# Kernel tuning notes

Hardware: AMD Instinct MI355X
Metric: run time of the kernel (lower is better)

## Reference

```python
import jax, jax.numpy as jnp
import numpy as np

B, S, DIM = 4, 2048, 1024
H, DH = 16, 64
INNER = H * DH  # 1024
SCALE = DH ** -0.5
NEG = -10000.0


def setup_inputs() -> dict:
    key = jax.random.key(0)
    k1, k2, k3, k4 = jax.random.split(key, 4)
    x = jax.random.normal(k1, (B, S, DIM), dtype=jnp.float32)
    w_qkv = jax.random.normal(k2, (DIM, 3 * INNER), dtype=jnp.float32) * (DIM ** -0.5)
    w_out = jax.random.normal(k3, (INNER, DIM), dtype=jnp.float32) * (INNER ** -0.5)
    b_out = jax.random.normal(k4, (DIM,), dtype=jnp.float32) * 0.01
    return {"x": x, "w_qkv": w_qkv, "w_out": w_out, "b_out": b_out}


def reference(x, w_qkv, w_out, b_out):
    b, s, _ = x.shape
    qkv = x @ w_qkv                                  # [b, s, 3*inner]
    q, k, v = jnp.split(qkv, 3, axis=-1)
    def heads(t):
        return t.reshape(b, s, H, DH).transpose(0, 2, 1, 3)  # [b, h, s, dh]
    q, k, v = heads(q), heads(k), heads(v)
    sim = jnp.einsum('bhid,bhjd->bhij', q, k)        # [b, h, s, s]
    i = jnp.arange(s)
    mask = jnp.where(i[None, :] <= i[:, None], 0.0, NEG).astype(sim.dtype)
    # NOTE: original scales (sim + mask), so mask bias is -10000*scale
    attn = jax.nn.softmax((sim + mask) * SCALE, axis=-1)
    out = jnp.einsum('bhij,bhjd->bhid', attn, v)     # [b, h, s, dh]
    out = out.transpose(0, 2, 1, 3).reshape(b, s, INNER)
    return out @ w_out + b_out
```

## Files before the change

kernel.cpp:

```cpp
#include <hip/hip_runtime.h>
#include <stdint.h>

typedef unsigned short u16;
typedef uint32_t u32;
typedef __attribute__((ext_vector_type(4))) float f32x4;
typedef __attribute__((ext_vector_type(16))) float f32x16;
typedef __attribute__((ext_vector_type(8))) short bf16x8;
typedef __attribute__((ext_vector_type(4))) u32 u32x4;

#define MFMA16(a,b,c) __builtin_amdgcn_mfma_f32_16x16x32_bf16((a),(b),(c),0,0,0)
#define MFMA32(a,b,c) __builtin_amdgcn_mfma_f32_32x32x16_bf16((a),(b),(c),0,0,0)
#define QSCALE 0.18033688011112042f
#define MASKB  -1803.3688011112042f
#define MBASE  -16.0f

__device__ __forceinline__ u16 f2bf(float f){
  union { float f; uint32_t u; } v; v.f = f;
  uint32_t r = v.u + 0x7fffu + ((v.u >> 16) & 1u);
  return (u16)(r >> 16);
}

__device__ __forceinline__ u32 cvtpk(float lo, float hi){
  u32 r;
  asm volatile("v_cvt_pk_bf16_f32 %0, %1, %2" : "=v"(r) : "v"(lo), "v"(hi));
  return r;
}

__device__ __forceinline__ void plswap(u32 &a, u32 &b){
  auto r = __builtin_amdgcn_permlane32_swap(a, b, false, false);
  union { decltype(r) v; u32 w[2]; } u; u.v = r;
  a = u.w[0]; b = u.w[1];
}

union U4 { u32x4 u; bf16x8 b; };
__device__ __forceinline__ bf16x8 mkfrag(u32 a, u32 b, u32 c, u32 d){
  U4 x; x.u = (u32x4){a,b,c,d}; return x.b;
}

__device__ __forceinline__ void gload16(const void* g, void* l){
  __builtin_amdgcn_global_load_lds(
      (const __attribute__((address_space(1))) void*)g,
      (__attribute__((address_space(3))) void*)l, 16, 0, 0);
}

__global__ __launch_bounds__(256) void cvt_bf16_k(const float* __restrict__ in, u16* __restrict__ out){
  int i = blockIdx.x*256 + threadIdx.x;
  float4 v = reinterpret_cast<const float4*>(in)[i];
  ushort4 o;
  o.x = f2bf(v.x); o.y = f2bf(v.y); o.z = f2bf(v.z); o.w = f2bf(v.w);
  reinterpret_cast<ushort4*>(out)[i] = o;
}

__global__ __launch_bounds__(256) void transpose_cvt_k(const float* __restrict__ in, u16* __restrict__ out,
                                                       int R, int C){
  __shared__ float tile[64][65];
  int c0 = blockIdx.x*64, r0 = blockIdx.y*64;
  int t = threadIdx.x; int cc = t & 63, rr = t >> 6;
  #pragma unroll
  for (int i=0;i<16;++i){ int r = rr + i*4; tile[r][cc] = in[(size_t)(r0+r)*C + c0+cc]; }
  __syncthreads();
  #pragma unroll
  for (int i=0;i<16;++i){ int r = rr + i*4; out[(size_t)(c0+r)*R + r0+cc] = f2bf(tile[cc][r]); }
}

__device__ __forceinline__ void gemm_core(const u16* __restrict__ A, const u16* __restrict__ Bt,
                                          int bm, int bn, char* lds, f32x4 (&acc)[4][4]){
  const int K = 1024;
  int tid = threadIdx.x, w = tid >> 6, l = tid & 63;
  int lrow = l & 15, lg = l >> 4;
  int wm = w >> 1, wn = w & 1;
  const u16* aSrc = A + (size_t)(bm*128 + w*32 + (l>>3))*K + (((l&7)^(l>>3))<<3);
  const u16* bSrc = Bt + (size_t)(bn*128 + w*32 + (l>>3))*K + (((l&7)^(l>>3))<<3);
  char* aDst = lds + w*4096;
  char* bDst = lds + 16384 + w*4096;
  for (int kk = 0; kk < 16; ++kk){
    __syncthreads();
    #pragma unroll
    for (int i=0;i<4;++i) gload16(aSrc + (size_t)i*8*K + kk*64, aDst + i*1024);
    #pragma unroll
    for (int i=0;i<4;++i) gload16(bSrc + (size_t)i*8*K + kk*64, bDst + i*1024);
    __syncthreads();
    #pragma unroll
    for (int ks=0; ks<2; ++ks){
      bf16x8 af[4], bfv[4];
      #pragma unroll
      for (int m=0;m<4;++m){
        int row = wm*64 + m*16 + lrow;
        af[m] = *reinterpret_cast<const bf16x8*>(lds + row*128 + (((ks*4+lg)^(row&7))<<4));
      }
      #pragma unroll
      for (int n=0;n<4;++n){
        int row = wn*64 + n*16 + lrow;
        bfv[n] = *reinterpret_cast<const bf16x8*>(lds + 16384 + row*128 + (((ks*4+lg)^(row&7))<<4));
      }
      #pragma unroll
      for (int m=0;m<4;++m){
        #pragma unroll
        for (int n=0;n<4;++n)
          acc[m][n] = MFMA16(af[m], bfv[n], acc[m][n]);
      }
    }
  }
}

__global__ __launch_bounds__(256,4) void gemm_qkv_k(const u16* __restrict__ A, const u16* __restrict__ Bt,
                                                    u16* __restrict__ qw, u16* __restrict__ kw,
                                                    u16* __restrict__ vtw){
  __shared__ __align__(16) char lds[32768];
  f32x4 acc[4][4];
  #pragma unroll
  for (int m=0;m<4;++m){
    #pragma unroll
    for (int n=0;n<4;++n) acc[m][n] = (f32x4){0.f,0.f,0.f,0.f};
  }
  int id = blockIdx.x + 24*blockIdx.y;
  int xcd = id & 7, s = id >> 3;
  int cb = s / 48, r = s % 48;
  int bm = xcd*8 + r/6;
  int bn = cb*6 + r%6;
  gemm_core(A, Bt, bm, bn, lds, acc);
  int tid = threadIdx.x, w = tid >> 6, l = tid & 63;
  int lrow = l & 15, lg = l >> 4;
  int wm = w >> 1, wn = w & 1;
  const int which = bn >> 3;
  if (which < 2){
    #pragma unroll
    for (int n=0;n<4;++n){
      int gcol = bn*128 + wn*64 + n*16 + lrow;
      int inner = gcol & 1023;
      int h = inner >> 6, d = inner & 63;
      #pragma unroll
      for (int m=0;m<4;++m){
        #pragma unroll
        for (int r2=0;r2<4;++r2){
          int grow = bm*128 + wm*64 + m*16 + lg*4 + r2;
          int b = grow >> 11, sq = grow & 2047;
          float v = acc[m][n][r2];
          if (which == 0)
            qw[((size_t)((b*16 + h)*2048 + sq))*64 + d] = f2bf(v * QSCALE);
          else
            kw[((size_t)((b*16 + h)*2048 + sq))*64 + d] = f2bf(v);
        }
      }
    }
  } else {
    __syncthreads();
    #pragma unroll
    for (int n=0;n<4;++n){
      int colL = wn*64 + n*16 + lrow;
      int swz = (colL & 7) << 4;
      #pragma unroll
      for (int m=0;m<4;++m){
        int rowL0 = wm*64 + m*16 + lg*4;
        ushort4 p;
        p.x = f2bf(acc[m][n][0]); p.y = f2bf(acc[m][n][1]);
        p.z = f2bf(acc[m][n][2]); p.w = f2bf(acc[m][n][3]);
        *reinterpret_cast<ushort4*>(lds + colL*256 + ((rowL0*2) ^ swz)) = p;
      }
    }
    __syncthreads();
    const int h0 = bn*2 - 32;
    const int grow0 = bm*128;
    const int b = grow0 >> 11, sq0 = grow0 & 2047;
    const int dp = tid >> 1;
    const int half = (tid & 1) * 128;
    const int h = h0 + (dp >> 6), d = dp & 63;
    const int swz = (dp & 7) << 4;
    u16* dst = vtw + ((size_t)((b*16 + h)*64 + d))*2048 + sq0 + half/2;
    #pragma unroll
    for (int i=0;i<8;++i){
      u32x4 v = *reinterpret_cast<const u32x4*>(lds + dp*256 + ((half + i*16) ^ swz));
      *reinterpret_cast<u32x4*>(dst + i*8) = v;
    }
  }
}

__global__ __launch_bounds__(256) void attn_k(const u16* __restrict__ Qw, const u16* __restrict__ Kw,
                                              const u16* __restrict__ VTw, u16* __restrict__ Ow){
  __shared__ __align__(16) char lds[32768];
  const int bh = blockIdx.x;
  const int y = blockIdx.y, yk = y >> 2, ya = y & 3;
  const int qb = (yk == 0) ? (15 - ya) : (yk == 1) ? (8 + ya) : (yk == 2) ? (4 + ya) : (3 - ya);
  const int tid = threadIdx.x, w = tid >> 6, l = tid & 63;
  const int lo = l & 31, hi = l >> 5;
  const size_t base = (size_t)bh * (2048*64);
  const int qw0 = qb*128 + w*32;
  const int q_l = qw0 + lo;

  bf16x8 qa[4];
  {
    const u16* qsrc = Qw + base + (size_t)q_l*64 + hi*8;
    #pragma unroll
    for (int ks=0; ks<4; ++ks) qa[ks] = *reinterpret_cast<const bf16x8*>(qsrc + ks*16);
  }

  const u32 ONE2 = 0x3F803F80u;
  const bf16x8 onesf = mkfrag(ONE2, ONE2, ONE2, ONE2);

  const int srow = tid >> 3;
  const int scs  = (tid & 7) ^ (srow & 7);
  const u16* kS = Kw  + base + (size_t)srow*64   + scs*8;
  const u16* vS = VTw + base + (size_t)srow*2048 + scs*8;

  f32x16 acc0 = {0,0,0,0,0,0,0,0,0,0,0,0,0,0,0,0};
  f32x16 acc1 = {0,0,0,0,0,0,0,0,0,0,0,0,0,0,0,0};
  f32x16 ls   = {0,0,0,0,0,0,0,0,0,0,0,0,0,0,0,0};
  const f32x16 minit = {MBASE,MBASE,MBASE,MBASE,MBASE,MBASE,MBASE,MBASE,
                        MBASE,MBASE,MBASE,MBASE,MBASE,MBASE,MBASE,MBASE};

  const int nt = qb*2 + 2;

  #define STAGE(buf, t) do { \
    int kv0_ = (t)*64; \
    gload16(kS + (size_t)kv0_*64,        lds + (buf)*16384 +     0 + w*1024); \
    gload16(kS + (size_t)(kv0_+32)*64,   lds + (buf)*16384 +  4096 + w*1024); \
    gload16(vS + kv0_,                   lds + (buf)*16384 +  8192 + w*1024); \
    gload16(vS + kv0_ + (size_t)32*2048, lds + (buf)*16384 + 12288 + w*1024); \
  } while(0)

  STAGE(0, 0);
  __syncthreads();

  int cur = 0;
  for (int t = 0; t < nt; ++t){
    if (t+1 < nt){
      if (cur) STAGE(0, t+1); else STAGE(1, t+1);
    }
    const int kv0 = t*64;
    const char* KB = lds + cur*16384;
    const char* VB = KB + 8192;
    if (kv0 + 63 <= qw0){
      f32x16 s0 = minit;
      f32x16 s1 = minit;
      __builtin_amdgcn_s_setprio(1);
      #pragma unroll
      for (int ks=0; ks<4; ++ks){
        int kr0 = lo, kr1 = 32 + lo;
        bf16x8 kf0 = *reinterpret_cast<const bf16x8*>(KB + kr0*128 + ((ks*32 + hi*16) ^ ((kr0&7)<<4)));
        bf16x8 kf1 = *reinterpret_cast<const bf16x8*>(KB + kr1*128 + ((ks*32 + hi*16) ^ ((kr1&7)<<4)));
        s0 = MFMA32(kf0, qa[ks], s0);
        s1 = MFMA32(kf1, qa[ks], s1);
      }
      __builtin_amdgcn_s_setprio(0);
      #pragma unroll
      for (int r=0; r<16; ++r) s0[r] = exp2f(s0[r]);
      #pragma unroll
      for (int r=0; r<16; ++r) s1[r] = exp2f(s1[r]);
      u32 wd0 = cvtpk(s0[0],s0[1]),   wd1 = cvtpk(s0[2],s0[3]);
      u32 wd2 = cvtpk(s0[4],s0[5]),   wd3 = cvtpk(s0[6],s0[7]);
      u32 wd4 = cvtpk(s0[8],s0[9]),   wd5 = cvtpk(s0[10],s0[11]);
      u32 wd6 = cvtpk(s0[12],s0[13]), wd7 = cvtpk(s0[14],s0[15]);
      u32 we0 = cvtpk(s1[0],s1[1]),   we1 = cvtpk(s1[2],s1[3]);
      u32 we2 = cvtpk(s1[4],s1[5]),   we3 = cvtpk(s1[6],s1[7]);
      u32 we4 = cvtpk(s1[8],s1[9]),   we5 = cvtpk(s1[10],s1[11]);
      u32 we6 = cvtpk(s1[12],s1[13]), we7 = cvtpk(s1[14],s1[15]);
      plswap(wd0, wd2); plswap(wd1, wd3); plswap(wd4, wd6); plswap(wd5, wd7);
      plswap(we0, we2); plswap(we1, we3); plswap(we4, we6); plswap(we5, we7);
      bf16x8 pf0 = mkfrag(wd0, wd1, wd2, wd3);
      bf16x8 pf1 = mkfrag(wd4, wd5, wd6, wd7);
      bf16x8 pf2 = mkfrag(we0, we1, we2, we3);
      bf16x8 pf3 = mkfrag(we4, we5, we6, we7);
      __builtin_amdgcn_s_setprio(1);
      {
        int vrow = lo;
        bf16x8 v0 = *reinterpret_cast<const bf16x8*>(VB + vrow*128 + ((      hi*16) ^ ((vrow&7)<<4)));
        bf16x8 v1 = *reinterpret_cast<const bf16x8*>(VB + vrow*128 + (( 32 + hi*16) ^ ((vrow&7)<<4)));
        bf16x8 v2 = *reinterpret_cast<const bf16x8*>(VB + vrow*128 + (( 64 + hi*16) ^ ((vrow&7)<<4)));
        bf16x8 v3 = *reinterpret_cast<const bf16x8*>(VB + vrow*128 + (( 96 + hi*16) ^ ((vrow&7)<<4)));
        acc0 = MFMA32(v0, pf0, acc0);
        acc0 = MFMA32(v1, pf1, acc0);
        acc0 = MFMA32(v2, pf2, acc0);
        acc0 = MFMA32(v3, pf3, acc0);
      }
      {
        int vrow = 32 + lo;
        bf16x8 v0 = *reinterpret_cast<const bf16x8*>(VB + vrow*128 + ((      hi*16) ^ ((vrow&7)<<4)));
        bf16x8 v1 = *reinterpret_cast<const bf16x8*>(VB + vrow*128 + (( 32 + hi*16) ^ ((vrow&7)<<4)));
        bf16x8 v2 = *reinterpret_cast<const bf16x8*>(VB + vrow*128 + (( 64 + hi*16) ^ ((vrow&7)<<4)));
        bf16x8 v3 = *reinterpret_cast<const bf16x8*>(VB + vrow*128 + (( 96 + hi*16) ^ ((vrow&7)<<4)));
        acc1 = MFMA32(v0, pf0, acc1);
        acc1 = MFMA32(v1, pf1, acc1);
        acc1 = MFMA32(v2, pf2, acc1);
        acc1 = MFMA32(v3, pf3, acc1);
      }
      ls = MFMA32(onesf, pf0, ls);
      ls = MFMA32(onesf, pf1, ls);
      ls = MFMA32(onesf, pf2, ls);
      ls = MFMA32(onesf, pf3, ls);
      __builtin_amdgcn_s_setprio(0);
    } else if (kv0 < qw0 + 32){
      #pragma unroll
      for (int t2=0; t2<2; ++t2){
        const int kvs0 = kv0 + t2*32;
        if (kvs0 < qw0 + 32){
          f32x16 s = minit;
          __builtin_amdgcn_s_setprio(1);
          #pragma unroll
          for (int ks=0; ks<4; ++ks){
            int krow = t2*32 + lo;
            bf16x8 kf = *reinterpret_cast<const bf16x8*>(KB + krow*128 + ((ks*32 + hi*16) ^ ((krow&7)<<4)));
            s = MFMA32(kf, qa[ks], s);
          }
          __builtin_amdgcn_s_setprio(0);
          if (kvs0 + 31 > qw0){
            #pragma unroll
            for (int r=0; r<16; ++r){
              int kvg = kvs0 + (r&3) + 8*(r>>2) + 4*hi;
              if (kvg > q_l) s[r] += MASKB;
            }
          }
          #pragma unroll
          for (int r=0; r<16; ++r) s[r] = exp2f(s[r]);
          u32 wd0 = cvtpk(s[0], s[1]),   wd1 = cvtpk(s[2], s[3]);
          u32 wd2 = cvtpk(s[4], s[5]),   wd3 = cvtpk(s[6], s[7]);
          u32 wd4 = cvtpk(s[8], s[9]),   wd5 = cvtpk(s[10], s[11]);
          u32 wd6 = cvtpk(s[12], s[13]), wd7 = cvtpk(s[14], s[15]);
          plswap(wd0, wd2); plswap(wd1, wd3);
          plswap(wd4, wd6); plswap(wd5, wd7);
          bf16x8 pf0 = mkfrag(wd0, wd1, wd2, wd3);
          bf16x8 pf1 = mkfrag(wd4, wd5, wd6, wd7);
          __builtin_amdgcn_s_setprio(1);
          {
            int vrow = lo;
            bf16x8 v0 = *reinterpret_cast<const bf16x8*>(VB + vrow*128 + ((t2*64 +      hi*16) ^ ((vrow&7)<<4)));
            bf16x8 v1 = *reinterpret_cast<const bf16x8*>(VB + vrow*128 + ((t2*64 + 32 + hi*16) ^ ((vrow&7)<<4)));
            acc0 = MFMA32(v0, pf0, acc0);
            acc0 = MFMA32(v1, pf1, acc0);
          }
          {
            int vrow = 32 + lo;
            bf16x8 v0 = *reinterpret_cast<const bf16x8*>(VB + vrow*128 + ((t2*64 +      hi*16) ^ ((vrow&7)<<4)));
            bf16x8 v1 = *reinterpret_cast<const bf16x8*>(VB + vrow*128 + ((t2*64 + 32 + hi*16) ^ ((vrow&7)<<4)));
            acc1 = MFMA32(v0, pf0, acc1);
            acc1 = MFMA32(v1, pf1, acc1);
          }
          ls = MFMA32(onesf, pf0, ls);
          ls = MFMA32(onesf, pf1, ls);
          __builtin_amdgcn_s_setprio(0);
        }
      }
    }
    __syncthreads();
    cur ^= 1;
  }
  #undef STAGE

  char* T = lds + w*4096;
  float inv = 1.0f / ls[0];
  #pragma unroll
  for (int i=0; i<8; ++i){
    int d = (2*i & 3) + 8*(2*i >> 2) + 4*hi;
    u32 wv0 = cvtpk(acc0[2*i]*inv, acc0[2*i+1]*inv);
    *reinterpret_cast<u32*>(T + lo*128 + ((d*2) ^ ((lo&7)<<4))) = wv0;
    u32 wv1 = cvtpk(acc1[2*i]*inv, acc1[2*i+1]*inv);
    *reinterpret_cast<u32*>(T + lo*128 + (((d+32)*2) ^ ((lo&7)<<4))) = wv1;
  }
  __syncthreads();
  const int b = bh >> 4, h = bh & 15;
  #pragma unroll
  for (int i=0; i<4; ++i){
    int q = i*8 + (l>>3), slot = l&7;
    bf16x8 v = *reinterpret_cast<const bf16x8*>(T + q*128 + ((slot*16) ^ ((q&7)<<4)));
    int sq = qb*128 + w*32 + q;
    *reinterpret_cast<bf16x8*>(Ow + ((size_t)(b*2048 + sq))*1024 + h*64 + slot*8) = v;
  }
}

__global__ __launch_bounds__(256,4) void gemm_out_k(const u16* __restrict__ A, const u16* __restrict__ Bt,
                                                    const float* __restrict__ bias_p, float* __restrict__ out){
  __shared__ __align__(16) char lds[32768];
  f32x4 acc[4][4];
  #pragma unroll
  for (int m=0;m<4;++m){
    #pragma unroll
    for (int n=0;n<4;++n) acc[m][n] = (f32x4){0.f,0.f,0.f,0.f};
  }
  int id = blockIdx.x + 8*blockIdx.y;
  int nid = (id & 7)*64 + (id >> 3);
  int bn = nid % 8, bm = nid / 8;
  gemm_core(A, Bt, bm, bn, lds, acc);
  int tid = threadIdx.x, w = tid >> 6, l = tid & 63;
  int lrow = l & 15, lg = l >> 4;
  int wm = w >> 1, wn = w & 1;
  #pragma unroll
  for (int n=0;n<4;++n){
    int gcol = bn*128 + wn*64 + n*16 + lrow;
    float bias = bias_p[gcol];
    #pragma unroll
    for (int m=0;m<4;++m){
      #pragma unroll
      for (int r=0;r<4;++r){
        int grow = bm*128 + wm*64 + m*16 + lg*4 + r;
        out[(size_t)grow*1024 + gcol] = acc[m][n][r] + bias;
      }
    }
  }
}

extern "C" void kernel_launch(void* const* d_in, const int* in_sizes, int n_in,
                              void* d_out, int out_size, void* d_ws, size_t ws_size,
                              hipStream_t stream){
  (void)in_sizes; (void)n_in; (void)out_size; (void)ws_size;
  const float* x     = (const float*)d_in[0];
  const float* w_qkv = (const float*)d_in[1];
  const float* w_out = (const float*)d_in[2];
  const float* b_out = (const float*)d_in[3];
  float* out = (float*)d_out;
  char* ws = (char*)d_ws;
  u16* xb    = (u16*)(ws + 0);
  u16* wqkvT = (u16*)(ws + 16777216);
  u16* woutT = (u16*)(ws + 23068672);
  u16* qw    = (u16*)(ws + 25165824);
  u16* kw    = (u16*)(ws + 41943040);
  u16* vtw   = (u16*)(ws + 58720256);
  u16* attn  = (u16*)(ws + 75497472);

  cvt_bf16_k<<<8192, 256, 0, stream>>>(x, xb);
  transpose_cvt_k<<<dim3(48,16), 256, 0, stream>>>(w_qkv, wqkvT, 1024, 3072);
  transpose_cvt_k<<<dim3(16,16), 256, 0, stream>>>(w_out, woutT, 1024, 1024);
  gemm_qkv_k<<<dim3(24,64), 256, 0, stream>>>(xb, wqkvT, qw, kw, vtw);
  attn_k<<<dim3(64,16), 256, 0, stream>>>(qw, kw, vtw, attn);
  gemm_out_k<<<dim3(8,64), 256, 0, stream>>>(attn, woutT, b_out, out);
}
```

Baseline: 172.0 us.

## Merge prep kernels, halve attention block size, raise QKV GEMM occupancy

Measured after the change: 182.3 us. +6.0%, slower.

```diff
diff --git a/kernel.cpp b/kernel.cpp
--- a/kernel.cpp
+++ b/kernel.cpp
@@ -43,19 +43,24 @@
       (__attribute__((address_space(3))) void*)l, 16, 0, 0);
 }
 
-__global__ __launch_bounds__(256) void cvt_bf16_k(const float* __restrict__ in, u16* __restrict__ out){
-  int i = blockIdx.x*256 + threadIdx.x;
-  float4 v = reinterpret_cast<const float4*>(in)[i];
-  ushort4 o;
-  o.x = f2bf(v.x); o.y = f2bf(v.y); o.z = f2bf(v.z); o.w = f2bf(v.w);
-  reinterpret_cast<ushort4*>(out)[i] = o;
-}
-
-__global__ __launch_bounds__(256) void transpose_cvt_k(const float* __restrict__ in, u16* __restrict__ out,
-                                                       int R, int C){
+__global__ __launch_bounds__(256) void prep_k(const float* __restrict__ x, u16* __restrict__ xb,
+                                              const float* __restrict__ w_qkv, u16* __restrict__ wqkvT,
+                                              const float* __restrict__ w_out, u16* __restrict__ woutT){
   __shared__ float tile[64][65];
-  int c0 = blockIdx.x*64, r0 = blockIdx.y*64;
-  int t = threadIdx.x; int cc = t & 63, rr = t >> 6;
+  const int id = blockIdx.x, t = threadIdx.x;
+  if (id < 8192){
+    int i = id*256 + t;
+    float4 v = reinterpret_cast<const float4*>(x)[i];
+    ushort4 o;
+    o.x = f2bf(v.x); o.y = f2bf(v.y); o.z = f2bf(v.z); o.w = f2bf(v.w);
+    reinterpret_cast<ushort4*>(xb)[i] = o;
+    return;
+  }
+  const float* in; u16* out; int R, C, bx, by;
+  if (id < 8960){ int id2 = id - 8192; in = w_qkv; out = wqkvT; R = 1024; C = 3072; bx = id2 % 48; by = id2 / 48; }
+  else          { int id3 = id - 8960; in = w_out; out = woutT; R = 1024; C = 1024; bx = id3 % 16; by = id3 / 16; }
+  int c0 = bx*64, r0 = by*64;
+  int cc = t & 63, rr = t >> 6;
   #pragma unroll
   for (int i=0;i<16;++i){ int r = rr + i*4; tile[r][cc] = in[(size_t)(r0+r)*C + c0+cc]; }
   __syncthreads();
@@ -103,7 +108,7 @@
   }
 }
 
-__global__ __launch_bounds__(256,4) void gemm_qkv_k(const u16* __restrict__ A, const u16* __restrict__ Bt,
+__global__ __launch_bounds__(256,5) void gemm_qkv_k(const u16* __restrict__ A, const u16* __restrict__ Bt,
                                                     u16* __restrict__ qw, u16* __restrict__ kw,
                                                     u16* __restrict__ vtw){
   __shared__ __align__(16) char lds[32768];
@@ -175,16 +180,15 @@
   }
 }
 
-__global__ __launch_bounds__(256) void attn_k(const u16* __restrict__ Qw, const u16* __restrict__ Kw,
+__global__ __launch_bounds__(128) void attn_k(const u16* __restrict__ Qw, const u16* __restrict__ Kw,
                                               const u16* __restrict__ VTw, u16* __restrict__ Ow){
   __shared__ __align__(16) char lds[32768];
   const int bh = blockIdx.x;
-  const int y = blockIdx.y, yk = y >> 2, ya = y & 3;
-  const int qb = (yk == 0) ? (15 - ya) : (yk == 1) ? (8 + ya) : (yk == 2) ? (4 + ya) : (3 - ya);
+  const int qb6 = 31 - blockIdx.y;
   const int tid = threadIdx.x, w = tid >> 6, l = tid & 63;
   const int lo = l & 31, hi = l >> 5;
   const size_t base = (size_t)bh * (2048*64);
-  const int qw0 = qb*128 + w*32;
+  const int qw0 = qb6*64 + w*32;
   const int q_l = qw0 + lo;
 
   bf16x8 qa[4];
@@ -197,10 +201,10 @@
   const u32 ONE2 = 0x3F803F80u;
   const bf16x8 onesf = mkfrag(ONE2, ONE2, ONE2, ONE2);
 
-  const int srow = tid >> 3;
-  const int scs  = (tid & 7) ^ (srow & 7);
-  const u16* kS = Kw  + base + (size_t)srow*64   + scs*8;
-  const u16* vS = VTw + base + (size_t)srow*2048 + scs*8;
+  const int srow8 = tid >> 3;
+  const int scs8  = (tid & 7) ^ (srow8 & 7);
+  const u16* kS = Kw  + base + (size_t)srow8*64   + scs8*8;
+  const u16* vS = VTw + base + (size_t)srow8*2048 + scs8*8;
 
   f32x16 acc0 = {0,0,0,0,0,0,0,0,0,0,0,0,0,0,0,0};
   f32x16 acc1 = {0,0,0,0,0,0,0,0,0,0,0,0,0,0,0,0};
@@ -208,14 +212,17 @@
   const f32x16 minit = {MBASE,MBASE,MBASE,MBASE,MBASE,MBASE,MBASE,MBASE,
                         MBASE,MBASE,MBASE,MBASE,MBASE,MBASE,MBASE,MBASE};
 
-  const int nt = qb*2 + 2;
+  const int nt = qb6 + 1;
 
   #define STAGE(buf, t) do { \
     int kv0_ = (t)*64; \
-    gload16(kS + (size_t)kv0_*64,        lds + (buf)*16384 +     0 + w*1024); \
-    gload16(kS + (size_t)(kv0_+32)*64,   lds + (buf)*16384 +  4096 + w*1024); \
-    gload16(vS + kv0_,                   lds + (buf)*16384 +  8192 + w*1024); \
-    gload16(vS + kv0_ + (size_t)32*2048, lds + (buf)*16384 + 12288 + w*1024); \
+    char* D_ = lds + (buf)*16384 + w*1024; \
+    _Pragma("unroll") \
+    for (int j=0;j<4;++j) \
+      gload16(kS + (size_t)(kv0_ + j*16)*64, D_ + j*2048); \
+    _Pragma("unroll") \
+    for (int j=0;j<4;++j) \
+      gload16(vS + (size_t)j*16*2048 + kv0_, D_ + 8192 + j*2048); \
   } while(0)
 
   STAGE(0, 0);
@@ -361,7 +368,7 @@
   for (int i=0; i<4; ++i){
     int q = i*8 + (l>>3), slot = l&7;
     bf16x8 v = *reinterpret_cast<const bf16x8*>(T + q*128 + ((slot*16) ^ ((q&7)<<4)));
-    int sq = qb*128 + w*32 + q;
+    int sq = qb6*64 + w*32 + q;
     *reinterpret_cast<bf16x8*>(Ow + ((size_t)(b*2048 + sq))*1024 + h*64 + slot*8) = v;
   }
 }
@@ -415,10 +422,8 @@
   u16* vtw   = (u16*)(ws + 58720256);
   u16* attn  = (u16*)(ws + 75497472);
 
-  cvt_bf16_k<<<8192, 256, 0, stream>>>(x, xb);
-  transpose_cvt_k<<<dim3(48,16), 256, 0, stream>>>(w_qkv, wqkvT, 1024, 3072);
-  transpose_cvt_k<<<dim3(16,16), 256, 0, stream>>>(w_out, woutT, 1024, 1024);
+  prep_k<<<9216, 256, 0, stream>>>(x, xb, w_qkv, wqkvT, w_out, woutT);
   gemm_qkv_k<<<dim3(24,64), 256, 0, stream>>>(xb, wqkvT, qw, kw, vtw);
-  attn_k<<<dim3(64,16), 256, 0, stream>>>(qw, kw, vtw, attn);
+  attn_k<<<dim3(64,32), 128, 0, stream>>>(qw, kw, vtw, attn);
   gemm_out_k<<<dim3(8,64), 256, 0, stream>>>(attn, woutT, b_out, out);
 }
```

## Merge prep kernels into one launch, add nontemporal stores, raise QKV occupancy

Applied to the files above, without the earlier changes.

Result: slower. 202.4 us (+17.7%).

```diff
diff --git a/kernel.cpp b/kernel.cpp
--- a/kernel.cpp
+++ b/kernel.cpp
@@ -43,19 +43,24 @@
       (__attribute__((address_space(3))) void*)l, 16, 0, 0);
 }
 
-__global__ __launch_bounds__(256) void cvt_bf16_k(const float* __restrict__ in, u16* __restrict__ out){
-  int i = blockIdx.x*256 + threadIdx.x;
-  float4 v = reinterpret_cast<const float4*>(in)[i];
-  ushort4 o;
-  o.x = f2bf(v.x); o.y = f2bf(v.y); o.z = f2bf(v.z); o.w = f2bf(v.w);
-  reinterpret_cast<ushort4*>(out)[i] = o;
-}
-
-__global__ __launch_bounds__(256) void transpose_cvt_k(const float* __restrict__ in, u16* __restrict__ out,
-                                                       int R, int C){
+__global__ __launch_bounds__(256) void prep_k(const float* __restrict__ x, u16* __restrict__ xb,
+                                              const float* __restrict__ w_qkv, u16* __restrict__ wqkvT,
+                                              const float* __restrict__ w_out, u16* __restrict__ woutT){
   __shared__ float tile[64][65];
-  int c0 = blockIdx.x*64, r0 = blockIdx.y*64;
-  int t = threadIdx.x; int cc = t & 63, rr = t >> 6;
+  const int id = blockIdx.x, t = threadIdx.x;
+  if (id < 8192){
+    int i = id*256 + t;
+    float4 v = reinterpret_cast<const float4*>(x)[i];
+    ushort4 o;
+    o.x = f2bf(v.x); o.y = f2bf(v.y); o.z = f2bf(v.z); o.w = f2bf(v.w);
+    reinterpret_cast<ushort4*>(xb)[i] = o;
+    return;
+  }
+  const float* in; u16* out; int R, C, bx, by;
+  if (id < 8960){ int id2 = id - 8192; in = w_qkv; out = wqkvT; R = 1024; C = 3072; bx = id2 % 48; by = id2 / 48; }
+  else          { int id3 = id - 8960; in = w_out; out = woutT; R = 1024; C = 1024; bx = id3 % 16; by = id3 / 16; }
+  int c0 = bx*64, r0 = by*64;
+  int cc = t & 63, rr = t >> 6;
   #pragma unroll
   for (int i=0;i<16;++i){ int r = rr + i*4; tile[r][cc] = in[(size_t)(r0+r)*C + c0+cc]; }
   __syncthreads();
@@ -103,7 +108,7 @@
   }
 }
 
-__global__ __launch_bounds__(256,4) void gemm_qkv_k(const u16* __restrict__ A, const u16* __restrict__ Bt,
+__global__ __launch_bounds__(256,5) void gemm_qkv_k(const u16* __restrict__ A, const u16* __restrict__ Bt,
                                                     u16* __restrict__ qw, u16* __restrict__ kw,
                                                     u16* __restrict__ vtw){
   __shared__ __align__(16) char lds[32768];
@@ -136,10 +141,9 @@
           int grow = bm*128 + wm*64 + m*16 + lg*4 + r2;
           int b = grow >> 11, sq = grow & 2047;
           float v = acc[m][n][r2];
-          if (which == 0)
-            qw[((size_t)((b*16 + h)*2048 + sq))*64 + d] = f2bf(v * QSCALE);
-          else
-            kw[((size_t)((b*16 + h)*2048 + sq))*64 + d] = f2bf(v);
+          u16 o = (which == 0) ? f2bf(v * QSCALE) : f2bf(v);
+          u16* dst = (which == 0) ? qw : kw;
+          __builtin_nontemporal_store(o, dst + ((size_t)((b*16 + h)*2048 + sq))*64 + d);
         }
       }
     }
@@ -170,7 +174,7 @@
     #pragma unroll
     for (int i=0;i<8;++i){
       u32x4 v = *reinterpret_cast<const u32x4*>(lds + dp*256 + ((half + i*16) ^ swz));
-      *reinterpret_cast<u32x4*>(dst + i*8) = v;
+      __builtin_nontemporal_store(v, reinterpret_cast<u32x4*>(dst + i*8));
     }
   }
 }
@@ -391,7 +395,7 @@
       #pragma unroll
       for (int r=0;r<4;++r){
         int grow = bm*128 + wm*64 + m*16 + lg*4 + r;
-        out[(size_t)grow*1024 + gcol] = acc[m][n][r] + bias;
+        __builtin_nontemporal_store(acc[m][n][r] + bias, out + (size_t)grow*1024 + gcol);
       }
     }
   }
@@ -415,9 +419,7 @@
   u16* vtw   = (u16*)(ws + 58720256);
   u16* attn  = (u16*)(ws + 75497472);
 
-  cvt_bf16_k<<<8192, 256, 0, stream>>>(x, xb);
-  transpose_cvt_k<<<dim3(48,16), 256, 0, stream>>>(w_qkv, wqkvT, 1024, 3072);
-  transpose_cvt_k<<<dim3(16,16), 256, 0, stream>>>(w_out, woutT, 1024, 1024);
+  prep_k<<<9216, 256, 0, stream>>>(x, xb, w_qkv, wqkvT, w_out, woutT);
   gemm_qkv_k<<<dim3(24,64), 256, 0, stream>>>(xb, wqkvT, qw, kw, vtw);
   attn_k<<<dim3(64,16), 256, 0, stream>>>(qw, kw, vtw, attn);
   gemm_out_k<<<dim3(8,64), 256, 0, stream>>>(attn, woutT, b_out, out);
```
